# Kernel tuning notes

Measured on AMD Instinct MI355X. Metric: run time of the kernel, lower is better.

## Reference

```python
import jax, jax.numpy as jnp
import numpy as np

B, N, C, O = 8, 4096, 256, 256  # batch, nodes, in_channels, out_channels
DENSITY = 0.01


def _cheb_k2(x_flat, A, W0, W1, b):
    """PyG ChebConv with K=2, sym normalization, lambda_max=2.
    Scaled Laplacian reduces to Lhat = -D^{-1/2} A D^{-1/2} (self-loops removed,
    diagonal of I - Ahat cancels with the fill_value=-1 self loops).
    Only the first N flattened nodes have edges (faithful to the source bug)."""
    n = A.shape[0]
    A = A * (1.0 - jnp.eye(n, dtype=A.dtype))  # remove_self_loops
    deg = A.sum(axis=1)                         # scatter(edge_weight, row)
    dis = jnp.where(deg > 0, jax.lax.rsqrt(jnp.where(deg > 0, deg, 1.0)), 0.0)
    Ahat = (dis[:, None] * A) * dis[None, :]    # D^{-1/2} A D^{-1/2}
    out = x_flat @ W0                           # Tx_0 term, all B*N nodes
    prop = -(Ahat @ x_flat[:n])                 # Tx_1 = Lhat x, first N nodes only
    out = out.at[:n].add(prop @ W1)
    return out + b


def setup_inputs() -> dict:
    key = jax.random.key(0)
    ks = jax.random.split(key, 12)
    x = jax.random.normal(ks[0], (B, N, C), jnp.float32)

    def adj(k):
        u = jax.random.uniform(k, (N, N), jnp.float32)
        return jnp.where(u < DENSITY, u, 0.0)

    adj1 = adj(ks[1])
    adj2 = adj(ks[2])
    s = 0.02
    Wc0_a = jax.random.normal(ks[3], (C, O), jnp.float32) * s
    Wc1_a = jax.random.normal(ks[4], (C, O), jnp.float32) * s
    bc_a = jnp.zeros((O,), jnp.float32)
    Wc0_b = jax.random.normal(ks[5], (C, O), jnp.float32) * s
    Wc1_b = jax.random.normal(ks[6], (C, O), jnp.float32) * s
    bc_b = jnp.zeros((O,), jnp.float32)
    Wp = jax.random.normal(ks[7], (2 * O, O), jnp.float32) * s  # [in,out] layout
    bp = jnp.zeros((O,), jnp.float32)
    return {"x": x, "adj1": adj1, "adj2": adj2,
            "Wc0_a": Wc0_a, "Wc1_a": Wc1_a, "bc_a": bc_a,
            "Wc0_b": Wc0_b, "Wc1_b": Wc1_b, "bc_b": bc_b,
            "Wp": Wp, "bp": bp}


def reference(x, adj1, adj2, Wc0_a, Wc1_a, bc_a, Wc0_b, Wc1_b, bc_b, Wp, bp):
    b, n, c = x.shape
    x_flat = x.reshape(-1, c)  # [B*N, C]
    o1 = _cheb_k2(x_flat, adj1, Wc0_a, Wc1_a, bc_a).reshape(b, n, -1)
    o2 = _cheb_k2(x_flat, adj2, Wc0_b, Wc1_b, bc_b).reshape(b, n, -1)
    out = jnp.concatenate([o1, o2], axis=-1)  # [B, N, 2*O]
    out = out @ Wp + bp                        # projection (dropout p=0)
    return out
```

## Files before the change

### kernel.cpp

```cpp
#include <hip/hip_runtime.h>
#include <hip/hip_bf16.h>
#include <stdint.h>

typedef __bf16 bf16;
typedef __attribute__((ext_vector_type(8))) __bf16 bf16x8;
typedef __attribute__((ext_vector_type(4))) float f32x4;


#define RCAP 96

__global__ __launch_bounds__(256, 4) void k_prep(const float* __restrict__ adj1,
                                                 const float* __restrict__ adj2,
                                                 const float* __restrict__ W0a,
                                                 const float* __restrict__ W1a,
                                                 const float* __restrict__ bca,
                                                 const float* __restrict__ W0b,
                                                 const float* __restrict__ W1b,
                                                 const float* __restrict__ bcb,
                                                 const float* __restrict__ Wp,
                                                 const float* __restrict__ bp,
                                                 float* __restrict__ dis,
                                                 int* __restrict__ ccnt,
                                                 uint2* __restrict__ cpair,
                                                 bf16* __restrict__ WxT,
                                                 bf16* __restrict__ WextT,
                                                 float* __restrict__ biasv) {
  int t = threadIdx.x;
  if (blockIdx.x < 256) {
    int c = blockIdx.x, o = t;
    const float* r0a = W0a + (size_t)c * 256;
    const float* r0b = W0b + (size_t)c * 256;
    const float* r1a = W1a + (size_t)c * 256;
    const float* r1b = W1b + (size_t)c * 256;
    float ax = 0.f, a1 = 0.f, a2 = 0.f, bacc = 0.f;
#pragma unroll 8
    for (int m = 0; m < 256; ++m) {
      float wpt = Wp[(size_t)m * 256 + o];
      float wpb = Wp[(size_t)(m + 256) * 256 + o];
      float wa = r0a[m], wb = r0b[m];
      float w1 = r1a[m], w2 = r1b[m];
      ax += wa * wpt + wb * wpb;
      a1 += w1 * wpt;
      a2 += w2 * wpb;
      bacc += bca[m] * wpt + bcb[m] * wpb;
    }
    WxT[(size_t)o * 256 + c] = (bf16)ax;
    WextT[(size_t)o * 512 + c] = (bf16)a1;
    WextT[(size_t)o * 512 + 256 + c] = (bf16)a2;
    if (c == 0) biasv[o] = bacc + bp[o];
    return;
  }
  int wave = t >> 6, lane = t & 63;
  int gw = (blockIdx.x - 256) * 4 + wave;
  int which = gw >> 12;
  int row = gw & 4095;
  const float* A = which ? adj2 : adj1;
  const f32x4* Arow = (const f32x4*)(A + (size_t)row * 4096);
  size_t base = (size_t)gw * RCAP;

  float s = 0.f;
  int wbase = 0;

  f32x4 cur[4];
#pragma unroll
  for (int q = 0; q < 4; ++q)
    cur[q] = __builtin_nontemporal_load(Arow + q * 64 + lane);

#pragma unroll
  for (int ch = 0; ch < 4; ++ch) {
    f32x4 nxt[4];
    if (ch < 3) {
#pragma unroll
      for (int q = 0; q < 4; ++q)
        nxt[q] = __builtin_nontemporal_load(Arow + ((ch + 1) * 4 + q) * 64 + lane);
    }
    int lcnt = 0;
#pragma unroll
    for (int q = 0; q < 4; ++q) {
      f32x4 v = cur[q];
      int j0 = (ch * 4 + q) * 256 + lane * 4;
#pragma unroll
      for (int k = 0; k < 4; ++k) {
        float f = v[k];
        if (f != 0.f && (j0 + k) != row) { s += f; ++lcnt; }
      }
    }
    int incl = lcnt;
#pragma unroll
    for (int off = 1; off < 64; off <<= 1) {
      int y = __shfl_up(incl, off, 64);
      if (lane >= off) incl += y;
    }
    int ctot = __shfl(incl, 63, 64);
    int pos = wbase + incl - lcnt;
#pragma unroll
    for (int q = 0; q < 4; ++q) {
      f32x4 v = cur[q];
      int j0 = (ch * 4 + q) * 256 + lane * 4;
#pragma unroll
      for (int k = 0; k < 4; ++k) {
        float f = v[k];
        int j = j0 + k;
        if (f != 0.f && j != row) {
          if (pos < RCAP) {
            uint2 pr;
            pr.x = (unsigned)j;
            pr.y = __float_as_uint(f);
            cpair[base + pos] = pr;
          }
          ++pos;
        }
      }
    }
    wbase += ctot;
    if (ch < 3) {
#pragma unroll
      for (int q = 0; q < 4; ++q) cur[q] = nxt[q];
    }
  }

#pragma unroll
  for (int off = 32; off >= 1; off >>= 1) s += __shfl_down(s, off, 64);
  if (lane == 0) {
    dis[gw] = (s > 0.f) ? (1.0f / sqrtf(s)) : 0.f;
    ccnt[gw] = (wbase > RCAP) ? RCAP : wbase;
  }
}

__global__ __launch_bounds__(256) void k_spmm2(const float* __restrict__ x,
                                               const float* __restrict__ dis,
                                               const int* __restrict__ ccnt,
                                               const uint2* __restrict__ cpair,
                                               bf16* __restrict__ P) {
  __shared__ float s_val[RCAP];
  __shared__ int s_idx[RCAP];
  int t = threadIdx.x;
  int row = blockIdx.x;
  int which = blockIdx.y;
  int r = (which << 12) | row;
  const float* dsel = dis + (which << 12);
  int n = ccnt[r];
  size_t base = (size_t)r * RCAP;
  if (t < n) {
    uint2 pr = cpair[base + t];
    int j = (int)pr.x;
    s_idx[t] = j;
    s_val[t] = __uint_as_float(pr.y) * dsel[j];
  }
  __syncthreads();
  float acc = 0.f;
  int e = 0;
  for (; e + 8 <= n; e += 8) {
    float v0 = x[(size_t)s_idx[e + 0] * 256 + t];
    float v1 = x[(size_t)s_idx[e + 1] * 256 + t];
    float v2 = x[(size_t)s_idx[e + 2] * 256 + t];
    float v3 = x[(size_t)s_idx[e + 3] * 256 + t];
    float v4 = x[(size_t)s_idx[e + 4] * 256 + t];
    float v5 = x[(size_t)s_idx[e + 5] * 256 + t];
    float v6 = x[(size_t)s_idx[e + 6] * 256 + t];
    float v7 = x[(size_t)s_idx[e + 7] * 256 + t];
    acc += s_val[e + 0] * v0 + s_val[e + 1] * v1 + s_val[e + 2] * v2 + s_val[e + 3] * v3 +
           s_val[e + 4] * v4 + s_val[e + 5] * v5 + s_val[e + 6] * v6 + s_val[e + 7] * v7;
  }
  for (; e + 4 <= n; e += 4) {
    float v0 = x[(size_t)s_idx[e + 0] * 256 + t];
    float v1 = x[(size_t)s_idx[e + 1] * 256 + t];
    float v2 = x[(size_t)s_idx[e + 2] * 256 + t];
    float v3 = x[(size_t)s_idx[e + 3] * 256 + t];
    acc += s_val[e + 0] * v0 + s_val[e + 1] * v1 + s_val[e + 2] * v2 + s_val[e + 3] * v3;
  }
  for (; e < n; ++e) acc += s_val[e] * x[(size_t)s_idx[e] * 256 + t];
  float prop = -dsel[row] * acc;
  P[(size_t)row * 512 + (size_t)which * 256 + t] = (bf16)prop;
}

__device__ __forceinline__ void mfma_tile(const char* ldsA, const char* ldsB,
                                          int wm, int wn, int lr, int quad,
                                          f32x4 acc[4][4]) {
  bf16x8 af[4], bb[4];
#pragma unroll
  for (int mf = 0; mf < 4; ++mf)
    af[mf] = *(const bf16x8*)(ldsA + ((wm * 64 + mf * 16 + lr) * 64 + quad * 16));
#pragma unroll
  for (int nf = 0; nf < 4; ++nf)
    bb[nf] = *(const bf16x8*)(ldsB + ((wn * 64 + nf * 16 + lr) * 64 + quad * 16));
#pragma unroll
  for (int mf = 0; mf < 4; ++mf)
#pragma unroll
    for (int nf = 0; nf < 4; ++nf)
      acc[mf][nf] = __builtin_amdgcn_mfma_f32_16x16x32_bf16(af[mf], bb[nf], acc[mf][nf], 0, 0, 0);
}

__global__ __launch_bounds__(256, 2) void k_gemm(const float* __restrict__ X,
                                                 const bf16* __restrict__ P,
                                                 const bf16* __restrict__ WxT,
                                                 const bf16* __restrict__ WextT,
                                                 const float* __restrict__ biasv,
                                                 float* __restrict__ out) {
  __shared__ __attribute__((aligned(16))) char ldsA[8192];
  __shared__ __attribute__((aligned(16))) char ldsB[8192];
  int t = threadIdx.x;
  int lane = t & 63, wave = t >> 6;
  int wm = wave & 1, wn = wave >> 1;
  int lr = lane & 15, quad = lane >> 4;
  int yy = blockIdx.y;
  int my = ((yy & 3) << 6) | (yy >> 2);
  int R0 = my * 128;
  int N0 = blockIdx.x * 128;

  f32x4 acc[4][4];
#pragma unroll
  for (int i = 0; i < 4; ++i)
#pragma unroll
    for (int j = 0; j < 4; ++j) acc[i][j] = (f32x4){0.f, 0.f, 0.f, 0.f};

  int srow = t >> 2;
  int scol = (t & 3) * 8;

  const float* xb0 = X + (size_t)(R0 + srow) * 256 + scol;
  const float* xb1 = X + (size_t)(R0 + srow + 64) * 256 + scol;
  const bf16* wb0 = WxT + (size_t)(N0 + srow) * 256 + scol;
  const bf16* wb1 = WxT + (size_t)(N0 + srow + 64) * 256 + scol;

  f32x4 f00 = *(const f32x4*)(xb0);
  f32x4 f01 = *(const f32x4*)(xb0 + 4);
  f32x4 f10 = *(const f32x4*)(xb1);
  f32x4 f11 = *(const f32x4*)(xb1 + 4);
  bf16x8 b0 = *(const bf16x8*)(wb0);
  bf16x8 b1 = *(const bf16x8*)(wb1);

#pragma unroll 1
  for (int step = 0; step < 8; ++step) {
    bf16x8 a0, a1;
#pragma unroll
    for (int k = 0; k < 4; ++k) {
      a0[k] = (bf16)f00[k]; a0[k + 4] = (bf16)f01[k];
      a1[k] = (bf16)f10[k]; a1[k + 4] = (bf16)f11[k];
    }
    __syncthreads();
    *(bf16x8*)(ldsA + t * 16) = a0;
    *(bf16x8*)(ldsA + 4096 + t * 16) = a1;
    *(bf16x8*)(ldsB + t * 16) = b0;
    *(bf16x8*)(ldsB + 4096 + t * 16) = b1;
    __syncthreads();
    if (step < 7) {
      int kb = (step + 1) * 32;
      f00 = *(const f32x4*)(xb0 + kb);
      f01 = *(const f32x4*)(xb0 + kb + 4);
      f10 = *(const f32x4*)(xb1 + kb);
      f11 = *(const f32x4*)(xb1 + kb + 4);
      b0 = *(const bf16x8*)(wb0 + kb);
      b1 = *(const bf16x8*)(wb1 + kb);
    }
    mfma_tile(ldsA, ldsB, wm, wn, lr, quad, acc);
  }

  if (R0 < 4096) {
    const bf16* pb0 = P + (size_t)(R0 + srow) * 512 + scol;
    const bf16* pb1 = P + (size_t)(R0 + srow + 64) * 512 + scol;
    const bf16* eb0 = WextT + (size_t)(N0 + srow) * 512 + scol;
    const bf16* eb1 = WextT + (size_t)(N0 + srow + 64) * 512 + scol;
    bf16x8 a0 = *(const bf16x8*)(pb0);
    bf16x8 a1 = *(const bf16x8*)(pb1);
    bf16x8 c0 = *(const bf16x8*)(eb0);
    bf16x8 c1 = *(const bf16x8*)(eb1);
#pragma unroll 1
    for (int step = 0; step < 16; ++step) {
      __syncthreads();
      *(bf16x8*)(ldsA + t * 16) = a0;
      *(bf16x8*)(ldsA + 4096 + t * 16) = a1;
      *(bf16x8*)(ldsB + t * 16) = c0;
      *(bf16x8*)(ldsB + 4096 + t * 16) = c1;
      __syncthreads();
      if (step < 15) {
        int kb = (step + 1) * 32;
        a0 = *(const bf16x8*)(pb0 + kb);
        a1 = *(const bf16x8*)(pb1 + kb);
        c0 = *(const bf16x8*)(eb0 + kb);
        c1 = *(const bf16x8*)(eb1 + kb);
      }
      mfma_tile(ldsA, ldsB, wm, wn, lr, quad, acc);
    }
  }

#pragma unroll
  for (int nf = 0; nf < 4; ++nf) {
    int ocol = N0 + wn * 64 + nf * 16 + lr;
    float bv = biasv[ocol];
#pragma unroll
    for (int mf = 0; mf < 4; ++mf) {
      int orow = R0 + wm * 64 + mf * 16 + quad * 4;
#pragma unroll
      for (int r = 0; r < 4; ++r)
        out[(size_t)(orow + r) * 256 + ocol] = acc[mf][nf][r] + bv;
    }
  }
}

extern "C" void kernel_launch(void* const* d_in, const int* in_sizes, int n_in,
                              void* d_out, int out_size, void* d_ws, size_t ws_size,
                              hipStream_t stream) {
  const float* x    = (const float*)d_in[0];
  const float* adj1 = (const float*)d_in[1];
  const float* adj2 = (const float*)d_in[2];
  const float* W0a  = (const float*)d_in[3];
  const float* W1a  = (const float*)d_in[4];
  const float* bca  = (const float*)d_in[5];
  const float* W0b  = (const float*)d_in[6];
  const float* W1b  = (const float*)d_in[7];
  const float* bcb  = (const float*)d_in[8];
  const float* Wp   = (const float*)d_in[9];
  const float* bp   = (const float*)d_in[10];
  float* out = (float*)d_out;

  char* ws = (char*)d_ws;
  float* dis   = (float*)(ws);
  float* biasv = (float*)(ws + 32 * 1024);
  bf16*  WxT   = (bf16*)(ws + 64 * 1024);
  bf16*  WextT = (bf16*)(ws + 320 * 1024);
  bf16*  P     = (bf16*)(ws + 704 * 1024);
  int*   ccnt  = (int*)(ws + 4800 * 1024);
  uint2* cpair = (uint2*)(ws + 4832 * 1024);

  k_prep<<<dim3(2304), dim3(256), 0, stream>>>(adj1, adj2, W0a, W1a, bca, W0b, W1b, bcb,
                                               Wp, bp, dis, ccnt, cpair,
                                               WxT, WextT, biasv);
  k_spmm2<<<dim3(4096, 2), dim3(256), 0, stream>>>(x, dis, ccnt, cpair, P);
  k_gemm<<<dim3(2, 256), dim3(256), 0, stream>>>(x, P, WxT, WextT, biasv, out);
}
```

Baseline: 231.0 us.

## Split propagation GEMM into separate kernel and drop prep prefetching

The extra K=512 propagation term for the first 4096 rows moves out of the main GEMM into a new k_prop kernel with 64x64 tiles that does a read-modify-write accumulate into out. This removes the load imbalance where only a quarter of the GEMM blocks ran the longer loop, and with it the row-swizzle that spread those blocks. In exchange it adds a launch and an extra read and write of part of the output. k_prep also drops its software-prefetch double buffer and lowers unroll to allow higher occupancy (launch bounds 8).

Measured after the change: 320.5 us. 38.7% more time.

```diff
diff --git a/kernel.cpp b/kernel.cpp
--- a/kernel.cpp
+++ b/kernel.cpp
@@ -9,7 +9,7 @@
 
 #define RCAP 96
 
-__global__ __launch_bounds__(256, 4) void k_prep(const float* __restrict__ adj1,
+__global__ __launch_bounds__(256, 8) void k_prep(const float* __restrict__ adj1,
                                                  const float* __restrict__ adj2,
                                                  const float* __restrict__ W0a,
                                                  const float* __restrict__ W1a,
@@ -33,7 +33,7 @@
     const float* r1a = W1a + (size_t)c * 256;
     const float* r1b = W1b + (size_t)c * 256;
     float ax = 0.f, a1 = 0.f, a2 = 0.f, bacc = 0.f;
-#pragma unroll 8
+#pragma unroll 4
     for (int m = 0; m < 256; ++m) {
       float wpt = Wp[(size_t)m * 256 + o];
       float wpb = Wp[(size_t)(m + 256) * 256 + o];
@@ -61,19 +61,12 @@
   float s = 0.f;
   int wbase = 0;
 
-  f32x4 cur[4];
-#pragma unroll
-  for (int q = 0; q < 4; ++q)
-    cur[q] = __builtin_nontemporal_load(Arow + q * 64 + lane);
-
 #pragma unroll
   for (int ch = 0; ch < 4; ++ch) {
-    f32x4 nxt[4];
-    if (ch < 3) {
-#pragma unroll
-      for (int q = 0; q < 4; ++q)
-        nxt[q] = __builtin_nontemporal_load(Arow + ((ch + 1) * 4 + q) * 64 + lane);
-    }
+    f32x4 cur[4];
+#pragma unroll
+    for (int q = 0; q < 4; ++q)
+      cur[q] = __builtin_nontemporal_load(Arow + (ch * 4 + q) * 64 + lane);
     int lcnt = 0;
 #pragma unroll
     for (int q = 0; q < 4; ++q) {
@@ -113,10 +106,6 @@
       }
     }
     wbase += ctot;
-    if (ch < 3) {
-#pragma unroll
-      for (int q = 0; q < 4; ++q) cur[q] = nxt[q];
-    }
   }
 
 #pragma unroll
@@ -192,9 +181,7 @@
 }
 
 __global__ __launch_bounds__(256, 2) void k_gemm(const float* __restrict__ X,
-                                                 const bf16* __restrict__ P,
                                                  const bf16* __restrict__ WxT,
-                                                 const bf16* __restrict__ WextT,
                                                  const float* __restrict__ biasv,
                                                  float* __restrict__ out) {
   __shared__ __attribute__((aligned(16))) char ldsA[8192];
@@ -203,9 +190,7 @@
   int lane = t & 63, wave = t >> 6;
   int wm = wave & 1, wn = wave >> 1;
   int lr = lane & 15, quad = lane >> 4;
-  int yy = blockIdx.y;
-  int my = ((yy & 3) << 6) | (yy >> 2);
-  int R0 = my * 128;
+  int R0 = blockIdx.y * 128;
   int N0 = blockIdx.x * 128;
 
   f32x4 acc[4][4];
@@ -255,34 +240,6 @@
     mfma_tile(ldsA, ldsB, wm, wn, lr, quad, acc);
   }
 
-  if (R0 < 4096) {
-    const bf16* pb0 = P + (size_t)(R0 + srow) * 512 + scol;
-    const bf16* pb1 = P + (size_t)(R0 + srow + 64) * 512 + scol;
-    const bf16* eb0 = WextT + (size_t)(N0 + srow) * 512 + scol;
-    const bf16* eb1 = WextT + (size_t)(N0 + srow + 64) * 512 + scol;
-    bf16x8 a0 = *(const bf16x8*)(pb0);
-    bf16x8 a1 = *(const bf16x8*)(pb1);
-    bf16x8 c0 = *(const bf16x8*)(eb0);
-    bf16x8 c1 = *(const bf16x8*)(eb1);
-#pragma unroll 1
-    for (int step = 0; step < 16; ++step) {
-      __syncthreads();
-      *(bf16x8*)(ldsA + t * 16) = a0;
-      *(bf16x8*)(ldsA + 4096 + t * 16) = a1;
-      *(bf16x8*)(ldsB + t * 16) = c0;
-      *(bf16x8*)(ldsB + 4096 + t * 16) = c1;
-      __syncthreads();
-      if (step < 15) {
-        int kb = (step + 1) * 32;
-        a0 = *(const bf16x8*)(pb0 + kb);
-        a1 = *(const bf16x8*)(pb1 + kb);
-        c0 = *(const bf16x8*)(eb0 + kb);
-        c1 = *(const bf16x8*)(eb1 + kb);
-      }
-      mfma_tile(ldsA, ldsB, wm, wn, lr, quad, acc);
-    }
-  }
-
 #pragma unroll
   for (int nf = 0; nf < 4; ++nf) {
     int ocol = N0 + wn * 64 + nf * 16 + lr;
@@ -293,6 +250,72 @@
 #pragma unroll
       for (int r = 0; r < 4; ++r)
         out[(size_t)(orow + r) * 256 + ocol] = acc[mf][nf][r] + bv;
+    }
+  }
+}
+
+__global__ __launch_bounds__(256, 2) void k_prop(const bf16* __restrict__ P,
+                                                 const bf16* __restrict__ WextT,
+                                                 float* __restrict__ out) {
+  __shared__ __attribute__((aligned(16))) char ldsA[4096];
+  __shared__ __attribute__((aligned(16))) char ldsB[4096];
+  int t = threadIdx.x;
+  int lane = t & 63, wave = t >> 6;
+  int wm = wave & 1, wn = wave >> 1;
+  int lr = lane & 15, quad = lane >> 4;
+  int R0 = blockIdx.y * 64;
+  int N0 = blockIdx.x * 64;
+
+  f32x4 acc[2][2];
+#pragma unroll
+  for (int i = 0; i < 2; ++i)
+#pragma unroll
+    for (int j = 0; j < 2; ++j) acc[i][j] = (f32x4){0.f, 0.f, 0.f, 0.f};
+
+  int srow = t >> 2;
+  int scol = (t & 3) * 8;
+
+  const bf16* pb = P + (size_t)(R0 + srow) * 512 + scol;
+  const bf16* eb = WextT + (size_t)(N0 + srow) * 512 + scol;
+  bf16x8 a0 = *(const bf16x8*)(pb);
+  bf16x8 b0 = *(const bf16x8*)(eb);
+
+#pragma unroll 1
+  for (int step = 0; step < 16; ++step) {
+    __syncthreads();
+    *(bf16x8*)(ldsA + t * 16) = a0;
+    *(bf16x8*)(ldsB + t * 16) = b0;
+    __syncthreads();
+    if (step < 15) {
+      int kb = (step + 1) * 32;
+      a0 = *(const bf16x8*)(pb + kb);
+      b0 = *(const bf16x8*)(eb + kb);
+    }
+    bf16x8 af[2], bf_[2];
+#pragma unroll
+    for (int mf = 0; mf < 2; ++mf)
+      af[mf] = *(const bf16x8*)(ldsA + ((wm * 32 + mf * 16 + lr) * 64 + quad * 16));
+#pragma unroll
+    for (int nf = 0; nf < 2; ++nf)
+      bf_[nf] = *(const bf16x8*)(ldsB + ((wn * 32 + nf * 16 + lr) * 64 + quad * 16));
+#pragma unroll
+    for (int mf = 0; mf < 2; ++mf)
+#pragma unroll
+      for (int nf = 0; nf < 2; ++nf)
+        acc[mf][nf] = __builtin_amdgcn_mfma_f32_16x16x32_bf16(af[mf], bf_[nf], acc[mf][nf], 0, 0, 0);
+  }
+
+#pragma unroll
+  for (int nf = 0; nf < 2; ++nf) {
+    int ocol = N0 + wn * 32 + nf * 16 + lr;
+#pragma unroll
+    for (int mf = 0; mf < 2; ++mf) {
+      int orow = R0 + wm * 32 + mf * 16 + quad * 4;
+#pragma unroll
+      for (int r = 0; r < 4; ++r) {
+        size_t idx = (size_t)(orow + r) * 256 + ocol;
+        out[idx] += acc[mf][nf][r];
+      }
     }
   }
 }
@@ -326,5 +349,6 @@
                                                Wp, bp, dis, ccnt, cpair,
                                                WxT, WextT, biasv);
   k_spmm2<<<dim3(4096, 2), dim3(256), 0, stream>>>(x, dis, ccnt, cpair, P);
-  k_gemm<<<dim3(2, 256), dim3(256), 0, stream>>>(x, P, WxT, WextT, biasv, out);
-}
+  k_gemm<<<dim3(2, 256), dim3(256), 0, stream>>>(x, WxT, biasv, out);
+  k_prop<<<dim3(4, 64), dim3(256), 0, stream>>>(P, WextT, out);
+}
```
